# Performance work log

Hardware: AMD Instinct MI355X
Metric: run time of the kernel (lower is better)

Reference implementation:

```python
import jax, jax.numpy as jnp
import numpy as np

SEQ_LEN = 8192
D_K = 128
NEG_BIG = 1000000000.0


def setup_inputs() -> dict:
    key = jax.random.key(0)
    kq, kk, kv = jax.random.split(key, 3)
    q = jax.random.normal(kq, (SEQ_LEN, D_K), dtype=jnp.float32)
    k = jax.random.normal(kk, (SEQ_LEN, D_K), dtype=jnp.float32)
    v = jax.random.normal(kv, (SEQ_LEN, D_K), dtype=jnp.float32)
    return {"q": q, "k": k, "v": v}


def reference(q, k, v):
    # q,k,v: (S, d). Naive attention with causal (look-ahead) mask, masked=True.
    d_k = q.shape[-1]
    scaled_logits = jnp.matmul(q, k.T) / jnp.sqrt(jnp.asarray(d_k, q.dtype))  # (S, S)
    look_ahead_mask = jnp.triu(jnp.ones((SEQ_LEN, SEQ_LEN), dtype=q.dtype), k=1)
    scaled_logits = scaled_logits - look_ahead_mask * NEG_BIG
    attn = jnp.matmul(jax.nn.softmax(scaled_logits, axis=-1), v)  # (S, d)
    return attn
```

## Files before the change

kernel.cpp:

```cpp
#include <hip/hip_runtime.h>
#include <hip/hip_bf16.h>
#include <math.h>

#define S_LEN 8192
#define DK    128
#define BM    64
#define BN    64
#define NQT   (S_LEN / BM)
#define SCALE2 (0.08838834764831845f * 1.4426950408889634f)

typedef __bf16 bf16x8_t __attribute__((ext_vector_type(8)));
typedef __bf16 bf16x4_t __attribute__((ext_vector_type(4)));
typedef float  floatx4  __attribute__((ext_vector_type(4)));

#define GLD16(g, l) __builtin_amdgcn_global_load_lds(                      \
    (const __attribute__((address_space(1))) void*)(g),                    \
    (__attribute__((address_space(3))) void*)(l), 16, 0, 0)

__device__ __forceinline__ float fexp2(float x) {
#if __has_builtin(__builtin_amdgcn_exp2f)
  return __builtin_amdgcn_exp2f(x);
#else
  return exp2f(x);
#endif
}

__global__ __launch_bounds__(256) void prep_kv(const float* __restrict__ K,
                                               const float* __restrict__ V,
                                               __bf16* __restrict__ Kb,
                                               __bf16* __restrict__ Vt) {
  __shared__ __bf16 t[64][DK + 8];
  const int bx  = blockIdx.x;
  const int tid = threadIdx.x;
  if (bx < (S_LEN * DK) / (256 * 4)) {
    const int i = (bx * 256 + tid) * 4;
    float4 v = *(const float4*)&K[i];
    bf16x4_t b;
    b[0] = (__bf16)v.x; b[1] = (__bf16)v.y; b[2] = (__bf16)v.z; b[3] = (__bf16)v.w;
    *(bf16x4_t*)&Kb[i] = b;
    return;
  }
  const int key0 = (bx - (S_LEN * DK) / (256 * 4)) * 64;
  {
    const int r = tid >> 2, cg = (tid & 3) * 32;
    const float* vp = V + (size_t)(key0 + r) * DK + cg;
    #pragma unroll
    for (int i = 0; i < 8; ++i) {
      float4 v = ((const float4*)vp)[i];
      bf16x4_t b;
      b[0] = (__bf16)v.x; b[1] = (__bf16)v.y; b[2] = (__bf16)v.z; b[3] = (__bf16)v.w;
      *(bf16x4_t*)&t[r][cg + i * 4] = b;
    }
  }
  __syncthreads();
  const int d = tid >> 1, h = (tid & 1) * 32;
  __bf16* op = Vt + (size_t)d * S_LEN + key0 + h;
  #pragma unroll
  for (int jb = 0; jb < 4; ++jb) {
    bf16x8_t b;
    #pragma unroll
    for (int j = 0; j < 8; ++j) b[j] = t[h + jb * 8 + j][d];
    *(bf16x8_t*)&op[jb * 8] = b;
  }
}

__global__ __launch_bounds__(256, 2)
void fa_part(const float* __restrict__ Q, const __bf16* __restrict__ Kb,
             const __bf16* __restrict__ Vtg, float* __restrict__ Opart,
             float* __restrict__ stats, int C, int direct) {
  __shared__ __align__(16) __bf16 Ks[2][BN * DK];
  __shared__ __align__(16) __bf16 Vts[BN * DK];
  __shared__ __align__(16) __bf16 Pl[4][16][BN + 8];

  const int tid  = threadIdx.x;
  const int wave = tid >> 6;
  const int lane = tid & 63;
  const int l15  = lane & 15;
  const int quad = lane >> 4;

  const int qtile = (NQT - 1) - blockIdx.x;
  const int g     = blockIdx.y;
  const int nt    = qtile + 1;
  const int ca    = qtile / C;
  if (g > ca) return;
  const int cr  = qtile - ca * C;
  const int jb0 = g * C;
  const int jb1 = (jb0 + C < nt) ? (jb0 + C) : nt;
  const int chunk = qtile + C * (ca * (ca - 1) / 2) + cr * ca + g;

  const int q0w = qtile * BM + wave * 16;

  bf16x8_t qf[4];
  {
    const float* qrow = Q + (size_t)(q0w + l15) * DK + quad * 8;
    #pragma unroll
    for (int kb = 0; kb < 4; ++kb) {
      const float4* p = (const float4*)(qrow + kb * 32);
      float4 a = p[0], b = p[1];
      bf16x8_t f;
      f[0]=(__bf16)a.x; f[1]=(__bf16)a.y; f[2]=(__bf16)a.z; f[3]=(__bf16)a.w;
      f[4]=(__bf16)b.x; f[5]=(__bf16)b.y; f[6]=(__bf16)b.z; f[7]=(__bf16)b.w;
      qf[kb] = f;
    }
  }

  const __bf16* kp[4]; const __bf16* vp[4]; int loff[4];
  {
    const int ck = l15 ^ ((wave * 4 + quad) & 15);
    const int cv = (lane & 7) ^ ((lane >> 3) & 7);
    #pragma unroll
    for (int t = 0; t < 4; ++t) {
      const int rk = t * 16 + wave * 4 + quad;
      kp[t] = Kb + ((size_t)(jb0 * BN + rk)) * DK + ck * 8;
      const int rv = t * 32 + wave * 8 + (lane >> 3);
      vp[t] = Vtg + (size_t)rv * S_LEN + jb0 * BN + cv * 8;
      loff[t] = t * 2048 + wave * 512;
    }
  }

  floatx4 o_acc[8];
  #pragma unroll
  for (int dt = 0; dt < 8; ++dt) o_acc[dt] = (floatx4){0.f, 0.f, 0.f, 0.f};
  float m_r[4], l_r[4];
  #pragma unroll
  for (int r = 0; r < 4; ++r) { m_r[r] = -INFINITY; l_r[r] = 0.f; }

  bf16x8_t onesf;
  #pragma unroll
  for (int j = 0; j < 8; ++j) onesf[j] = (__bf16)1.0f;

  #pragma unroll
  for (int t = 0; t < 4; ++t) { GLD16(kp[t], &Ks[0][loff[t]]); kp[t] += BN * DK; }
  __syncthreads();

  int bsel = 0;
  for (int jb = jb0; jb < jb1; ++jb) {
    if (jb + 1 < jb1) {
      #pragma unroll
      for (int t = 0; t < 4; ++t) { GLD16(kp[t], &Ks[bsel ^ 1][loff[t]]); kp[t] += BN * DK; }
    }
    #pragma unroll
    for (int t = 0; t < 4; ++t) { GLD16(vp[t], &Vts[loff[t]]); vp[t] += BN; }

    const __bf16* Kcur = Ks[bsel];

    floatx4 sv[4];
    __builtin_amdgcn_s_setprio(1);
    #pragma unroll
    for (int n = 0; n < 4; ++n) {
      floatx4 acc = (floatx4){0.f, 0.f, 0.f, 0.f};
      #pragma unroll
      for (int kb = 0; kb < 4; ++kb) {
        bf16x8_t bfr = *(const bf16x8_t*)
            &Kcur[(n * 16 + l15) * DK + (((kb * 4 + quad) ^ l15) * 8)];
        acc = __builtin_amdgcn_mfma_f32_16x16x32_bf16(qf[kb], bfr, acc, 0, 0, 0);
      }
      sv[n] = acc;
    }
    __builtin_amdgcn_s_setprio(0);

    if (jb == qtile) {
      #pragma unroll
      for (int n = 0; n < 4; ++n) {
        const int key = jb * BN + n * 16 + l15;
        #pragma unroll
        for (int r = 0; r < 4; ++r) {
          const int qi = q0w + quad * 4 + r;
          const float vv = sv[n][r] * SCALE2;
          sv[n][r] = (key > qi) ? -1e30f : vv;
        }
      }
    } else {
      #pragma unroll
      for (int n = 0; n < 4; ++n)
        #pragma unroll
        for (int r = 0; r < 4; ++r) sv[n][r] *= SCALE2;
    }

    float rm[4];
    #pragma unroll
    for (int r = 0; r < 4; ++r)
      rm[r] = fmaxf(fmaxf(sv[0][r], sv[1][r]), fmaxf(sv[2][r], sv[3][r]));
    #pragma unroll
    for (int off = 8; off >= 1; off >>= 1) {
      #pragma unroll
      for (int r = 0; r < 4; ++r) rm[r] = fmaxf(rm[r], __shfl_xor(rm[r], off));
    }

    const int grow = (rm[0] > m_r[0]) || (rm[1] > m_r[1]) ||
                     (rm[2] > m_r[2]) || (rm[3] > m_r[3]);
    if (__any(grow)) {
      float al[4];
      #pragma unroll
      for (int r = 0; r < 4; ++r) {
        const float mn = fmaxf(m_r[r], rm[r]);
        al[r] = fexp2(m_r[r] - mn);
        m_r[r] = mn;
        l_r[r] *= al[r];
      }
      #pragma unroll
      for (int dt = 0; dt < 8; ++dt)
        #pragma unroll
        for (int r = 0; r < 4; ++r) o_acc[dt][r] *= al[r];
    }

    #pragma unroll
    for (int n = 0; n < 4; ++n)
      #pragma unroll
      for (int r = 0; r < 4; ++r)
        Pl[wave][quad * 4 + r][n * 16 + l15] = (__bf16)fexp2(sv[n][r] - m_r[r]);

    __syncthreads();

    floatx4 lacc = (floatx4){0.f, 0.f, 0.f, 0.f};
    __builtin_amdgcn_s_setprio(1);
    #pragma unroll
    for (int kc = 0; kc < 2; ++kc) {
      bf16x8_t af = *(const bf16x8_t*)&Pl[wave][l15][kc * 32 + quad * 8];
      lacc = __builtin_amdgcn_mfma_f32_16x16x32_bf16(af, onesf, lacc, 0, 0, 0);
      #pragma unroll
      for (int dt = 0; dt < 8; ++dt) {
        bf16x8_t vf = *(const bf16x8_t*)
            &Vts[(dt * 16 + l15) * BN + (((kc * 4 + quad) ^ (l15 & 7)) * 8)];
        o_acc[dt] = __builtin_amdgcn_mfma_f32_16x16x32_bf16(af, vf, o_acc[dt], 0, 0, 0);
      }
    }
    __builtin_amdgcn_s_setprio(0);
    #pragma unroll
    for (int r = 0; r < 4; ++r) l_r[r] += lacc[r];

    __syncthreads();
    bsel ^= 1;
  }

  if (direct) {
    #pragma unroll
    for (int r = 0; r < 4; ++r) {
      const float inv = 1.0f / l_r[r];
      float* orow = Opart + (size_t)(q0w + quad * 4 + r) * DK + l15;
      #pragma unroll
      for (int dt = 0; dt < 8; ++dt) orow[dt * 16] = o_acc[dt][r] * inv;
    }
  } else {
    #pragma unroll
    for (int r = 0; r < 4; ++r) {
      const int row = wave * 16 + quad * 4 + r;
      float* orow = Opart + ((size_t)chunk * BM + row) * DK + l15;
      #pragma unroll
      for (int dt = 0; dt < 8; ++dt) orow[dt * 16] = o_acc[dt][r];
    }
    if (l15 == 0) {
      #pragma unroll
      for (int r = 0; r < 4; ++r) {
        const int row = wave * 16 + quad * 4 + r;
        stats[((size_t)chunk * BM + row) * 2 + 0] = m_r[r];
        stats[((size_t)chunk * BM + row) * 2 + 1] = l_r[r];
      }
    }
  }
}

__global__ __launch_bounds__(256)
void fa_reduce(const float* __restrict__ Opart, const float* __restrict__ stats,
               float* __restrict__ O, int C) {
  const int wave = threadIdx.x >> 6, lane = threadIdx.x & 63;
  const int row = blockIdx.x * 4 + wave;
  const int qt = row >> 6, r = row & 63;

  const int ca = qt / C, cr = qt - ca * C;
  const int base = qt + C * (ca * (ca - 1) / 2) + cr * ca;
  const int nch = ca + 1;

  float M = -INFINITY;
  for (int g = 0; g < nch; ++g)
    M = fmaxf(M, stats[((size_t)(base + g) * BM + r) * 2]);

  float L = 0.f, ax = 0.f, ay = 0.f;
  for (int g = 0; g < nch; ++g) {
    const size_t sidx = (size_t)(base + g) * BM + r;
    const float m = stats[sidx * 2];
    const float w = fexp2(m - M);
    L += stats[sidx * 2 + 1] * w;
    float2 o = *(const float2*)&Opart[sidx * DK + lane * 2];
    ax += w * o.x; ay += w * o.y;
  }
  const float inv = 1.f / L;
  float2 res; res.x = ax * inv; res.y = ay * inv;
  *(float2*)&O[(size_t)row * DK + lane * 2] = res;
}

extern "C" void kernel_launch(void* const* d_in, const int* in_sizes, int n_in,
                              void* d_out, int out_size, void* d_ws, size_t ws_size,
                              hipStream_t stream) {
  (void)in_sizes; (void)n_in; (void)out_size;
  const float* q = (const float*)d_in[0];
  const float* k = (const float*)d_in[1];
  const float* v = (const float*)d_in[2];
  float* out = (float*)d_out;

  const size_t conv_bytes = (size_t)S_LEN * DK * 2 * 2;
  const size_t per_chunk  = (size_t)(BM * DK + 2 * BM) * 4;

  int C = 0; long long nc = 0;
  for (int c = 8; c <= NQT; ++c) {
    const int a = NQT / c, rr = NQT % c;
    const long long n = (long long)NQT + (long long)c * a * (a - 1) / 2 +
                        (long long)rr * a;
    if (conv_bytes + (size_t)n * per_chunk <= ws_size) { C = c; nc = n; break; }
  }

  __bf16* Kb = (__bf16*)d_ws;
  __bf16* Vt = Kb + (size_t)S_LEN * DK;

  prep_kv<<<(S_LEN * DK) / (256 * 4) + S_LEN / 64, 256, 0, stream>>>(k, v, Kb, Vt);

  if (C) {
    float* Opart = (float*)(Vt + (size_t)S_LEN * DK);
    float* stats = Opart + (size_t)nc * BM * DK;
    const int gy = (NQT - 1) / C + 1;
    fa_part<<<dim3(NQT, gy), 256, 0, stream>>>(q, Kb, Vt, Opart, stats, C, 0);
    fa_reduce<<<S_LEN / 4, 256, 0, stream>>>(Opart, stats, out, C);
  } else {
    fa_part<<<dim3(NQT, 1), 256, 0, stream>>>(q, Kb, Vt, out, out, NQT, 1);
  }
}
```

Baseline: 136.6 us.

## Switch flash attention to 32x32x16 MFMA with 128-row query tiles and register-resident P

Doubles the query tile to 128 rows, with each wave owning 32 queries, and moves from 16x16x32 to 32x32x16 bf16 MFMA in a transposed S^T = K·Q^T form. Each lane then holds one query's scores, so the row max and sum need only a permlane32 swap instead of shuffle trees. P is packed to bf16 and rearranged in registers rather than written to LDS, removing the P buffer and one barrier per step. V is now double-buffered alongside K, the softmax scale is folded into Q at load, and the chunk split and reduce indexing are reworked for the new tile sizes. The larger tiles and accumulators raise register pressure, which may cost occupancy, and the diagonal tiles do more masked work.

```diff
diff --git a/kernel.cpp b/kernel.cpp
--- a/kernel.cpp
+++ b/kernel.cpp
@@ -4,14 +4,16 @@
 
 #define S_LEN 8192
 #define DK    128
-#define BM    64
+#define BM    128
 #define BN    64
 #define NQT   (S_LEN / BM)
 #define SCALE2 (0.08838834764831845f * 1.4426950408889634f)
 
 typedef __bf16 bf16x8_t __attribute__((ext_vector_type(8)));
 typedef __bf16 bf16x4_t __attribute__((ext_vector_type(4)));
-typedef float  floatx4  __attribute__((ext_vector_type(4)));
+typedef __bf16 bf16x2_t __attribute__((ext_vector_type(2)));
+typedef float  floatx16 __attribute__((ext_vector_type(16)));
+typedef unsigned uintx4 __attribute__((ext_vector_type(4)));
 
 #define GLD16(g, l) __builtin_amdgcn_global_load_lds(                      \
     (const __attribute__((address_space(1))) void*)(g),                    \
@@ -22,6 +24,26 @@
   return __builtin_amdgcn_exp2f(x);
 #else
   return exp2f(x);
+#endif
+}
+
+__device__ __forceinline__ unsigned pack2(float a, float b) {
+  bf16x2_t w; w[0] = (__bf16)a; w[1] = (__bf16)b;
+  return __builtin_bit_cast(unsigned, w);
+}
+
+__device__ __forceinline__ void xswap(unsigned &x, unsigned &y) {
+#if __has_builtin(__builtin_amdgcn_permlane32_swap)
+  typedef unsigned v2u __attribute__((ext_vector_type(2)));
+  v2u t = __builtin_amdgcn_permlane32_swap(x, y, false, false);
+  x = t[0]; y = t[1];
+#else
+  const unsigned sx = (unsigned)__shfl_xor((int)x, 32);
+  const unsigned sy = (unsigned)__shfl_xor((int)y, 32);
+  const bool lo = ((threadIdx.x & 63) < 32);
+  const unsigned nx = lo ? x : sy;
+  const unsigned ny = lo ? sx : y;
+  x = nx; y = ny;
 #endif
 }
 
@@ -69,48 +91,50 @@
              const __bf16* __restrict__ Vtg, float* __restrict__ Opart,
              float* __restrict__ stats, int C, int direct) {
   __shared__ __align__(16) __bf16 Ks[2][BN * DK];
-  __shared__ __align__(16) __bf16 Vts[BN * DK];
-  __shared__ __align__(16) __bf16 Pl[4][16][BN + 8];
+  __shared__ __align__(16) __bf16 Vts[2][DK * BN];
 
   const int tid  = threadIdx.x;
   const int wave = tid >> 6;
   const int lane = tid & 63;
-  const int l15  = lane & 15;
-  const int quad = lane >> 4;
+  const int l31  = lane & 31;
+  const int hh   = lane >> 5;
 
   const int qtile = (NQT - 1) - blockIdx.x;
   const int g     = blockIdx.y;
-  const int nt    = qtile + 1;
-  const int ca    = qtile / C;
-  if (g > ca) return;
-  const int cr  = qtile - ca * C;
-  const int jb0 = g * C;
+  const int nt    = 2 * qtile + 2;
+  const int jb0   = g * C;
+  if (jb0 >= nt) return;
   const int jb1 = (jb0 + C < nt) ? (jb0 + C) : nt;
-  const int chunk = qtile + C * (ca * (ca - 1) / 2) + cr * ca + g;
-
-  const int q0w = qtile * BM + wave * 16;
-
-  bf16x8_t qf[4];
+  const int h2 = C >> 1;
+  const int ca = qtile / h2, cr = qtile - ca * h2;
+  const int chunk = h2 * ca * (ca + 1) / 2 + cr * (ca + 1) + g;
+
+  const int qw  = qtile * BM + wave * 32;
+  const int myq = qw + l31;
+
+  bf16x8_t qf[8];
   {
-    const float* qrow = Q + (size_t)(q0w + l15) * DK + quad * 8;
-    #pragma unroll
-    for (int kb = 0; kb < 4; ++kb) {
-      const float4* p = (const float4*)(qrow + kb * 32);
-      float4 a = p[0], b = p[1];
+    const float* qrow = Q + (size_t)myq * DK + hh * 8;
+    #pragma unroll
+    for (int s = 0; s < 8; ++s) {
+      float4 x = *(const float4*)(qrow + s * 16);
+      float4 y = *(const float4*)(qrow + s * 16 + 4);
       bf16x8_t f;
-      f[0]=(__bf16)a.x; f[1]=(__bf16)a.y; f[2]=(__bf16)a.z; f[3]=(__bf16)a.w;
-      f[4]=(__bf16)b.x; f[5]=(__bf16)b.y; f[6]=(__bf16)b.z; f[7]=(__bf16)b.w;
-      qf[kb] = f;
+      f[0]=(__bf16)(x.x*SCALE2); f[1]=(__bf16)(x.y*SCALE2);
+      f[2]=(__bf16)(x.z*SCALE2); f[3]=(__bf16)(x.w*SCALE2);
+      f[4]=(__bf16)(y.x*SCALE2); f[5]=(__bf16)(y.y*SCALE2);
+      f[6]=(__bf16)(y.z*SCALE2); f[7]=(__bf16)(y.w*SCALE2);
+      qf[s] = f;
     }
   }
 
   const __bf16* kp[4]; const __bf16* vp[4]; int loff[4];
   {
-    const int ck = l15 ^ ((wave * 4 + quad) & 15);
+    const int ck = (lane & 15) ^ ((wave * 4 + (lane >> 4)) & 15);
     const int cv = (lane & 7) ^ ((lane >> 3) & 7);
     #pragma unroll
     for (int t = 0; t < 4; ++t) {
-      const int rk = t * 16 + wave * 4 + quad;
+      const int rk = t * 16 + wave * 4 + (lane >> 4);
       kp[t] = Kb + ((size_t)(jb0 * BN + rk)) * DK + ck * 8;
       const int rv = t * 32 + wave * 8 + (lane >> 3);
       vp[t] = Vtg + (size_t)rv * S_LEN + jb0 * BN + cv * 8;
@@ -118,144 +142,159 @@
     }
   }
 
-  floatx4 o_acc[8];
+  floatx16 o_acc[4];
   #pragma unroll
-  for (int dt = 0; dt < 8; ++dt) o_acc[dt] = (floatx4){0.f, 0.f, 0.f, 0.f};
-  float m_r[4], l_r[4];
-  #pragma unroll
-  for (int r = 0; r < 4; ++r) { m_r[r] = -INFINITY; l_r[r] = 0.f; }
-
-  bf16x8_t onesf;
-  #pragma unroll
-  for (int j = 0; j < 8; ++j) onesf[j] = (__bf16)1.0f;
+  for (int d = 0; d < 4; ++d)
+    #pragma unroll
+    for (int r = 0; r < 16; ++r) o_acc[d][r] = 0.f;
+  float m_r = -INFINITY, l_r = 0.f;
 
   #pragma unroll
   for (int t = 0; t < 4; ++t) { GLD16(kp[t], &Ks[0][loff[t]]); kp[t] += BN * DK; }
+  #pragma unroll
+  for (int t = 0; t < 4; ++t) { GLD16(vp[t], &Vts[0][loff[t]]); vp[t] += BN; }
   __syncthreads();
 
-  int bsel = 0;
+  int cur = 0;
   for (int jb = jb0; jb < jb1; ++jb) {
     if (jb + 1 < jb1) {
       #pragma unroll
-      for (int t = 0; t < 4; ++t) { GLD16(kp[t], &Ks[bsel ^ 1][loff[t]]); kp[t] += BN * DK; }
-    }
-    #pragma unroll
-    for (int t = 0; t < 4; ++t) { GLD16(vp[t], &Vts[loff[t]]); vp[t] += BN; }
-
-    const __bf16* Kcur = Ks[bsel];
-
-    floatx4 sv[4];
-    __builtin_amdgcn_s_setprio(1);
-    #pragma unroll
-    for (int n = 0; n < 4; ++n) {
-      floatx4 acc = (floatx4){0.f, 0.f, 0.f, 0.f};
-      #pragma unroll
-      for (int kb = 0; kb < 4; ++kb) {
-        bf16x8_t bfr = *(const bf16x8_t*)
-            &Kcur[(n * 16 + l15) * DK + (((kb * 4 + quad) ^ l15) * 8)];
-        acc = __builtin_amdgcn_mfma_f32_16x16x32_bf16(qf[kb], bfr, acc, 0, 0, 0);
-      }
-      sv[n] = acc;
-    }
-    __builtin_amdgcn_s_setprio(0);
-
-    if (jb == qtile) {
-      #pragma unroll
-      for (int n = 0; n < 4; ++n) {
-        const int key = jb * BN + n * 16 + l15;
-        #pragma unroll
-        for (int r = 0; r < 4; ++r) {
-          const int qi = q0w + quad * 4 + r;
-          const float vv = sv[n][r] * SCALE2;
-          sv[n][r] = (key > qi) ? -1e30f : vv;
+      for (int t = 0; t < 4; ++t) { GLD16(kp[t], &Ks[cur ^ 1][loff[t]]); kp[t] += BN * DK; }
+      #pragma unroll
+      for (int t = 0; t < 4; ++t) { GLD16(vp[t], &Vts[cur ^ 1][loff[t]]); vp[t] += BN; }
+    }
+
+    if (jb * 64 <= qw + 31) {
+      const __bf16* Kc = Ks[cur];
+      const __bf16* Vc = Vts[cur];
+
+      floatx16 sv[2];
+      __builtin_amdgcn_s_setprio(1);
+      #pragma unroll
+      for (int g1 = 0; g1 < 2; ++g1) {
+        floatx16 acc;
+        #pragma unroll
+        for (int r = 0; r < 16; ++r) acc[r] = 0.f;
+        const int row = g1 * 32 + l31;
+        #pragma unroll
+        for (int s = 0; s < 8; ++s) {
+          bf16x8_t kf = *(const bf16x8_t*)
+              &Kc[row * DK + (((s * 2 + hh) ^ (row & 15)) * 8)];
+          acc = __builtin_amdgcn_mfma_f32_32x32x16_bf16(kf, qf[s], acc, 0, 0, 0);
         }
-      }
-    } else {
-      #pragma unroll
-      for (int n = 0; n < 4; ++n)
-        #pragma unroll
-        for (int r = 0; r < 4; ++r) sv[n][r] *= SCALE2;
-    }
-
-    float rm[4];
-    #pragma unroll
-    for (int r = 0; r < 4; ++r)
-      rm[r] = fmaxf(fmaxf(sv[0][r], sv[1][r]), fmaxf(sv[2][r], sv[3][r]));
-    #pragma unroll
-    for (int off = 8; off >= 1; off >>= 1) {
-      #pragma unroll
-      for (int r = 0; r < 4; ++r) rm[r] = fmaxf(rm[r], __shfl_xor(rm[r], off));
-    }
-
-    const int grow = (rm[0] > m_r[0]) || (rm[1] > m_r[1]) ||
-                     (rm[2] > m_r[2]) || (rm[3] > m_r[3]);
-    if (__any(grow)) {
-      float al[4];
-      #pragma unroll
-      for (int r = 0; r < 4; ++r) {
-        const float mn = fmaxf(m_r[r], rm[r]);
-        al[r] = fexp2(m_r[r] - mn);
-        m_r[r] = mn;
-        l_r[r] *= al[r];
-      }
-      #pragma unroll
-      for (int dt = 0; dt < 8; ++dt)
-        #pragma unroll
-        for (int r = 0; r < 4; ++r) o_acc[dt][r] *= al[r];
-    }
-
-    #pragma unroll
-    for (int n = 0; n < 4; ++n)
-      #pragma unroll
-      for (int r = 0; r < 4; ++r)
-        Pl[wave][quad * 4 + r][n * 16 + l15] = (__bf16)fexp2(sv[n][r] - m_r[r]);
+        sv[g1] = acc;
+      }
+      __builtin_amdgcn_s_setprio(0);
+
+      if (jb * 64 + 63 > qw) {
+        #pragma unroll
+        for (int g1 = 0; g1 < 2; ++g1)
+          #pragma unroll
+          for (int r = 0; r < 16; ++r) {
+            const int key = jb * 64 + g1 * 32 + (r & 3) + ((r >> 2) << 3) + (hh << 2);
+            if (key > myq) sv[g1][r] = -1e30f;
+          }
+      }
+
+      float pm = sv[0][0];
+      #pragma unroll
+      for (int g1 = 0; g1 < 2; ++g1)
+        #pragma unroll
+        for (int r = 0; r < 16; ++r) pm = fmaxf(pm, sv[g1][r]);
+      {
+        unsigned b0 = __builtin_bit_cast(unsigned, pm), b1 = b0;
+        xswap(b0, b1);
+        pm = fmaxf(__builtin_bit_cast(float, b0), __builtin_bit_cast(float, b1));
+      }
+      const int grow = (pm > m_r) ? 1 : 0;
+      if (__any(grow)) {
+        const float mn = fmaxf(m_r, pm);
+        const float al = fexp2(m_r - mn);
+        m_r = mn; l_r *= al;
+        #pragma unroll
+        for (int d = 0; d < 4; ++d)
+          #pragma unroll
+          for (int r = 0; r < 16; ++r) o_acc[d][r] *= al;
+      }
+
+      float rs = 0.f;
+      #pragma unroll
+      for (int g1 = 0; g1 < 2; ++g1)
+        #pragma unroll
+        for (int r = 0; r < 16; ++r) {
+          const float pv = fexp2(sv[g1][r] - m_r);
+          sv[g1][r] = pv;
+          rs += pv;
+        }
+      {
+        unsigned b0 = __builtin_bit_cast(unsigned, rs), b1 = b0;
+        xswap(b0, b1);
+        l_r += __builtin_bit_cast(float, b0) + __builtin_bit_cast(float, b1);
+      }
+
+      unsigned pk[4][4];
+      #pragma unroll
+      for (int g1 = 0; g1 < 2; ++g1) {
+        unsigned W0 = pack2(sv[g1][0],  sv[g1][1]);
+        unsigned W1 = pack2(sv[g1][2],  sv[g1][3]);
+        unsigned W2 = pack2(sv[g1][4],  sv[g1][5]);
+        unsigned W3 = pack2(sv[g1][6],  sv[g1][7]);
+        unsigned W4 = pack2(sv[g1][8],  sv[g1][9]);
+        unsigned W5 = pack2(sv[g1][10], sv[g1][11]);
+        unsigned W6 = pack2(sv[g1][12], sv[g1][13]);
+        unsigned W7 = pack2(sv[g1][14], sv[g1][15]);
+        xswap(W0, W2); xswap(W1, W3);
+        xswap(W4, W6); xswap(W5, W7);
+        pk[g1*2+0][0]=W0; pk[g1*2+0][1]=W1; pk[g1*2+0][2]=W2; pk[g1*2+0][3]=W3;
+        pk[g1*2+1][0]=W4; pk[g1*2+1][1]=W5; pk[g1*2+1][2]=W6; pk[g1*2+1][3]=W7;
+      }
+
+      __builtin_amdgcn_s_setprio(1);
+      #pragma unroll
+      for (int ks = 0; ks < 4; ++ks) {
+        uintx4 u; u[0]=pk[ks][0]; u[1]=pk[ks][1]; u[2]=pk[ks][2]; u[3]=pk[ks][3];
+        const bf16x8_t pf = __builtin_bit_cast(bf16x8_t, u);
+        #pragma unroll
+        for (int d = 0; d < 4; ++d) {
+          const int row = d * 32 + l31;
+          bf16x8_t vf = *(const bf16x8_t*)
+              &Vc[row * BN + (((ks * 2 + hh) ^ (row & 7)) * 8)];
+          o_acc[d] = __builtin_amdgcn_mfma_f32_32x32x16_bf16(vf, pf, o_acc[d], 0, 0, 0);
+        }
+      }
+      __builtin_amdgcn_s_setprio(0);
+    }
 
     __syncthreads();
-
-    floatx4 lacc = (floatx4){0.f, 0.f, 0.f, 0.f};
-    __builtin_amdgcn_s_setprio(1);
-    #pragma unroll
-    for (int kc = 0; kc < 2; ++kc) {
-      bf16x8_t af = *(const bf16x8_t*)&Pl[wave][l15][kc * 32 + quad * 8];
-      lacc = __builtin_amdgcn_mfma_f32_16x16x32_bf16(af, onesf, lacc, 0, 0, 0);
-      #pragma unroll
-      for (int dt = 0; dt < 8; ++dt) {
-        bf16x8_t vf = *(const bf16x8_t*)
-            &Vts[(dt * 16 + l15) * BN + (((kc * 4 + quad) ^ (l15 & 7)) * 8)];
-        o_acc[dt] = __builtin_amdgcn_mfma_f32_16x16x32_bf16(af, vf, o_acc[dt], 0, 0, 0);
-      }
-    }
-    __builtin_amdgcn_s_setprio(0);
-    #pragma unroll
-    for (int r = 0; r < 4; ++r) l_r[r] += lacc[r];
-
-    __syncthreads();
-    bsel ^= 1;
+    cur ^= 1;
   }
 
   if (direct) {
-    #pragma unroll
-    for (int r = 0; r < 4; ++r) {
-      const float inv = 1.0f / l_r[r];
-      float* orow = Opart + (size_t)(q0w + quad * 4 + r) * DK + l15;
-      #pragma unroll
-      for (int dt = 0; dt < 8; ++dt) orow[dt * 16] = o_acc[dt][r] * inv;
-    }
+    const float inv = 1.0f / l_r;
+    float* orow = Opart + (size_t)myq * DK;
+    #pragma unroll
+    for (int d = 0; d < 4; ++d)
+      #pragma unroll
+      for (int mI = 0; mI < 4; ++mI) {
+        float4 st;
+        st.x = o_acc[d][mI*4+0] * inv; st.y = o_acc[d][mI*4+1] * inv;
+        st.z = o_acc[d][mI*4+2] * inv; st.w = o_acc[d][mI*4+3] * inv;
+        *(float4*)&orow[d * 32 + mI * 8 + hh * 4] = st;
+      }
   } else {
-    #pragma unroll
-    for (int r = 0; r < 4; ++r) {
-      const int row = wave * 16 + quad * 4 + r;
-      float* orow = Opart + ((size_t)chunk * BM + row) * DK + l15;
-      #pragma unroll
-      for (int dt = 0; dt < 8; ++dt) orow[dt * 16] = o_acc[dt][r];
-    }
-    if (l15 == 0) {
-      #pragma unroll
-      for (int r = 0; r < 4; ++r) {
-        const int row = wave * 16 + quad * 4 + r;
-        stats[((size_t)chunk * BM + row) * 2 + 0] = m_r[r];
-        stats[((size_t)chunk * BM + row) * 2 + 1] = l_r[r];
-      }
+    float* orow = Opart + ((size_t)chunk * BM + wave * 32 + l31) * DK;
+    #pragma unroll
+    for (int d = 0; d < 4; ++d)
+      #pragma unroll
+      for (int mI = 0; mI < 4; ++mI) {
+        float4 st;
+        st.x = o_acc[d][mI*4+0]; st.y = o_acc[d][mI*4+1];
+        st.z = o_acc[d][mI*4+2]; st.w = o_acc[d][mI*4+3];
+        *(float4*)&orow[d * 32 + mI * 8 + hh * 4] = st;
+      }
+    if (hh == 0) {
+      stats[((size_t)chunk * BM + wave * 32 + l31) * 2 + 0] = m_r;
+      stats[((size_t)chunk * BM + wave * 32 + l31) * 2 + 1] = l_r;
     }
   }
 }
@@ -265,11 +304,12 @@
                float* __restrict__ O, int C) {
   const int wave = threadIdx.x >> 6, lane = threadIdx.x & 63;
   const int row = blockIdx.x * 4 + wave;
-  const int qt = row >> 6, r = row & 63;
-
-  const int ca = qt / C, cr = qt - ca * C;
-  const int base = qt + C * (ca * (ca - 1) / 2) + cr * ca;
-  const int nch = ca + 1;
+  const int qt = row >> 7, r = row & 127;
+
+  const int h2 = C >> 1;
+  const int ca = qt / h2, cr = qt - ca * h2;
+  const int base = h2 * ca * (ca + 1) / 2 + cr * (ca + 1);
+  const int nch = (qt + h2) / h2;
 
   float M = -INFINITY;
   for (int g = 0; g < nch; ++g)
@@ -302,10 +342,10 @@
   const size_t per_chunk  = (size_t)(BM * DK + 2 * BM) * 4;
 
   int C = 0; long long nc = 0;
-  for (int c = 8; c <= NQT; ++c) {
-    const int a = NQT / c, rr = NQT % c;
-    const long long n = (long long)NQT + (long long)c * a * (a - 1) / 2 +
-                        (long long)rr * a;
+  for (int c = 8; c <= 2 * NQT; c += 2) {
+    const int h2 = c / 2;
+    const int a = NQT / h2, rr = NQT - a * h2;
+    const long long n = (long long)h2 * a * (a + 1) / 2 + (long long)rr * (a + 1);
     if (conv_bytes + (size_t)n * per_chunk <= ws_size) { C = c; nc = n; break; }
   }
 
@@ -317,10 +357,10 @@
   if (C) {
     float* Opart = (float*)(Vt + (size_t)S_LEN * DK);
     float* stats = Opart + (size_t)nc * BM * DK;
-    const int gy = (NQT - 1) / C + 1;
+    const int gy = (2 * NQT + C - 1) / C;
     fa_part<<<dim3(NQT, gy), 256, 0, stream>>>(q, Kb, Vt, Opart, stats, C, 0);
     fa_reduce<<<S_LEN / 4, 256, 0, stream>>>(Opart, stats, out, C);
   } else {
-    fa_part<<<dim3(NQT, 1), 256, 0, stream>>>(q, Kb, Vt, out, out, NQT, 1);
-  }
-}
+    fa_part<<<dim3(NQT, 1), 256, 0, stream>>>(q, Kb, Vt, out, out, 2 * NQT, 1);
+  }
+}
```

Result: faster. 124.2 us (-9.1%).
